# Kernel optimization log

Hardware: AMD Instinct MI355X
Metric: run time of the kernel (lower is better)

## Reference

```python
import jax, jax.numpy as jnp
import numpy as np

EPS_BN = 1e-5
K_NN = 5


def _curvature(x, k=K_NN):
    # x: [B, P, 3] -> concat inverse mean kNN distance -> [B, P, 4]
    def per_sample(pts):  # [P, 3]
        sq = jnp.sum(pts * pts, axis=1)
        d2 = sq[:, None] + sq[None, :] - 2.0 * (pts @ pts.T)
        dist = jnp.sqrt(jnp.maximum(d2, 0.0))  # [P, P], matches torch.cdist p=2
        neg_vals, _ = jax.lax.top_k(-dist, k + 1)  # k+1 smallest distances
        dists = -neg_vals[:, 1:]  # drop self (distance 0)
        dmean = jnp.mean(dists, axis=1, keepdims=True)  # [P, 1]
        return 1.0 / (1e-8 + dmean)
    curv = jax.vmap(per_sample)(x)  # [B, P, 1]
    return jnp.concatenate([x, curv], axis=2)


def _bn(h, g, b, axes):
    # BatchNorm (training mode, batch statistics), biased variance like torch
    m = jnp.mean(h, axis=axes, keepdims=True)
    v = jnp.var(h, axis=axes, keepdims=True)
    return (h - m) / jnp.sqrt(v + EPS_BN) * g + b


def setup_inputs() -> dict:
    key = jax.random.key(0)
    ks = jax.random.split(key, 16)
    B, P, OUTDIM = 32, 2048, 40

    def rn(k, shape, scale=0.05):
        return jax.random.normal(k, shape, dtype=jnp.float32) * scale

    return {
        "x": jax.random.normal(ks[0], (B, P, 3), dtype=jnp.float32),
        # 1x1 Conv1d weights stored as [out_ch, in_ch]
        "conv1_w": rn(ks[1], (64, 4)), "conv1_b": rn(ks[2], (64,)),
        "bn1_g": jnp.ones((64,), jnp.float32), "bn1_b": jnp.zeros((64,), jnp.float32),
        "conv2_w": rn(ks[3], (128, 64)), "conv2_b": rn(ks[4], (128,)),
        "bn2_g": jnp.ones((128,), jnp.float32), "bn2_b": jnp.zeros((128,), jnp.float32),
        "conv3_w": rn(ks[5], (1024, 128)), "conv3_b": rn(ks[6], (1024,)),
        "bn3_g": jnp.ones((1024,), jnp.float32), "bn3_b": jnp.zeros((1024,), jnp.float32),
        "fc1_w": rn(ks[7], (512, 1024)), "fc1_b": rn(ks[8], (512,)),
        "bnf1_g": jnp.ones((512,), jnp.float32), "bnf1_b": jnp.zeros((512,), jnp.float32),
        "fc2_w": rn(ks[9], (256, 512)), "fc2_b": rn(ks[10], (256,)),
        "bnf2_g": jnp.ones((256,), jnp.float32), "bnf2_b": jnp.zeros((256,), jnp.float32),
        # outdim separate Linear(256,1) layers stacked into one [OUTDIM, 256] matrix
        "out_w": rn(ks[11], (OUTDIM, 256)), "out_b": rn(ks[12], (OUTDIM,)),
    }


def reference(x, conv1_w, conv1_b, bn1_g, bn1_b, conv2_w, conv2_b, bn2_g, bn2_b,
              conv3_w, conv3_b, bn3_g, bn3_b, fc1_w, fc1_b, bnf1_g, bnf1_b,
              fc2_w, fc2_b, bnf2_g, bnf2_b, out_w, out_b):
    h = _curvature(x)  # [B, P, 4]
    # feature_layer1: Conv1d(4,64,1)+BN+ReLU; 1x1 conv == per-point matmul
    h = jax.nn.relu(_bn(h @ conv1_w.T + conv1_b, bn1_g, bn1_b, (0, 1)))
    # feature_layer2: Conv1d(64,128,1)+BN+ReLU, Conv1d(128,1024,1)+BN+ReLU
    h = jax.nn.relu(_bn(h @ conv2_w.T + conv2_b, bn2_g, bn2_b, (0, 1)))
    h = jax.nn.relu(_bn(h @ conv3_w.T + conv3_b, bn3_g, bn3_b, (0, 1)))
    h = jnp.max(h, axis=1)  # global max pool over points -> [B, 1024]
    # shared_layer
    h = jax.nn.relu(_bn(h @ fc1_w.T + fc1_b, bnf1_g, bnf1_b, (0,)))
    h = jax.nn.relu(_bn(h @ fc2_w.T + fc2_b, bnf2_g, bnf2_b, (0,)))
    logits = h @ out_w.T + out_b  # concatenated per-class Linear(256,1) heads
    return jax.nn.log_softmax(logits, axis=1)
```

## Files before the change

kernel.cpp:

```cpp
#include <hip/hip_runtime.h>
#include <hip/hip_bf16.h>
#include <math.h>

#define EPS_BN 1e-5f

constexpr int BATCH = 32;
constexpr int NPTS  = 2048;
constexpr int BP    = BATCH * NPTS;

using s16x8 = __attribute__((ext_vector_type(8))) short;
using u32x4 = __attribute__((ext_vector_type(4))) unsigned;
using f32x4 = __attribute__((ext_vector_type(4))) float;

static __device__ __forceinline__ unsigned short f2bf(float f) {
  union { float f; unsigned u; } x{f};
  unsigned r = x.u + 0x7fffu + ((x.u >> 16) & 1u);
  return (unsigned short)(r >> 16);
}
static __device__ __forceinline__ float bf2f(unsigned short s) {
  union { unsigned u; float f; } x;
  x.u = ((unsigned)s) << 16;
  return x.f;
}
static __device__ __forceinline__ unsigned pk2bf(float lo, float hi) {
  __hip_bfloat162 t = __float22bfloat162_rn(float2{lo, hi});
  unsigned r;
  __builtin_memcpy(&r, &t, 4);
  return r;
}

static __device__ __forceinline__ void gload_lds16(const void* g, void* l) {
  __builtin_amdgcn_global_load_lds((const __attribute__((address_space(1))) void*)g,
                                   (__attribute__((address_space(3))) void*)l, 16, 0, 0);
}

static __device__ __forceinline__ float wave_reduce_add(float v) {
#pragma unroll
  for (int off = 32; off > 0; off >>= 1) v += __shfl_xor(v, off);
  return v;
}

static __device__ __forceinline__ void ins6(float (&nn)[6], float c) {
  float b0 = fminf(nn[0], c);
  float b1 = __builtin_amdgcn_fmed3f(c, nn[1], nn[0]);
  float b2 = __builtin_amdgcn_fmed3f(c, nn[2], nn[1]);
  float b3 = __builtin_amdgcn_fmed3f(c, nn[3], nn[2]);
  float b4 = __builtin_amdgcn_fmed3f(c, nn[4], nn[3]);
  float b5 = __builtin_amdgcn_fmed3f(c, nn[5], nn[4]);
  nn[0] = b0; nn[1] = b1; nn[2] = b2; nn[3] = b3; nn[4] = b4; nn[5] = b5;
}

constexpr int CHP = 257;
__global__ __launch_bounds__(256) void curv1_kernel(const float* __restrict__ x,
                                                    const float* __restrict__ c1w,
                                                    const float* __restrict__ c1b,
                                                    unsigned short* __restrict__ z1bf,
                                                    float* __restrict__ part) {
  __shared__ float4 pts[8 * CHP];
  __shared__ float wT[4 * 64], lb1[64], sfeat[32 * 4];
  __shared__ float ls[256], lq[256];
  int b = blockIdx.y;
  const float* xb = x + (size_t)b * NPTS * 3;
  int tid = threadIdx.x;
  {
    int k = tid >> 6, c = tid & 63;
    wT[k * 64 + c] = c1w[c * 4 + k];
    if (tid < 64) lb1[tid] = c1b[tid];
  }
#pragma unroll
  for (int k = 0; k < 8; k++) {
    int i = k * 256 + tid;
    float qx = xb[i * 3 + 0], qy = xb[i * 3 + 1], qz = xb[i * 3 + 2];
    pts[k * CHP + tid] = make_float4(qx, qy, qz, 0.5f * (qx * qx + qy * qy + qz * qz));
  }
  __syncthreads();
  int row = blockIdx.x * 32 + (tid >> 3);
  int sub = tid & 7;
  float4 p = pts[(row >> 8) * CHP + (row & 255)];
  float px = p.x, py = p.y, pz = p.z;
  float nn[6];
#pragma unroll
  for (int j = 0; j < 6; j++) nn[j] = 3.4e38f;
  const float4* cp = pts + sub * CHP;
  for (int j = 0; j < 256; j += 4) {
    float4 q0 = cp[j + 0], q1 = cp[j + 1], q2 = cp[j + 2], q3 = cp[j + 3];
    ins6(nn, fmaf(-px, q0.x, fmaf(-py, q0.y, fmaf(-pz, q0.z, q0.w))));
    ins6(nn, fmaf(-px, q1.x, fmaf(-py, q1.y, fmaf(-pz, q1.z, q1.w))));
    ins6(nn, fmaf(-px, q2.x, fmaf(-py, q2.y, fmaf(-pz, q2.z, q2.w))));
    ins6(nn, fmaf(-px, q3.x, fmaf(-py, q3.y, fmaf(-pz, q3.z, q3.w))));
  }
#pragma unroll
  for (int m = 1; m <= 4; m <<= 1) {
    float other[6];
#pragma unroll
    for (int k = 0; k < 6; k++) other[k] = __shfl_xor(nn[k], m);
#pragma unroll
    for (int k = 0; k < 6; k++) ins6(nn, other[k]);
  }
  if (sub == 0) {
    float p2 = px * px + py * py + pz * pz;
    float dm = 0.f;
#pragma unroll
    for (int i = 1; i < 6; i++) dm += sqrtf(fmaxf(fmaf(2.f, nn[i], p2), 0.f));
    dm *= 0.2f;
    float curv = 1.0f / (1e-8f + dm);
    int lr = tid >> 3;
    sfeat[lr * 4 + 0] = px;
    sfeat[lr * 4 + 1] = py;
    sfeat[lr * 4 + 2] = pz;
    sfeat[lr * 4 + 3] = curv;
  }
  __syncthreads();
  {
    int c = tid & 63, rg = tid >> 6;
    float w0 = wT[c], w1 = wT[64 + c], w2v = wT[128 + c], w3 = wT[192 + c];
    float bb = lb1[c];
    int growbase = b * NPTS + blockIdx.x * 32;
    float s = 0.f, q = 0.f;
#pragma unroll
    for (int i = 0; i < 8; i++) {
      int lr = rg * 8 + i;
      float4 f = *(const float4*)(sfeat + lr * 4);
      float acc = bb + f.x * w0 + f.y * w1 + f.z * w2v + f.w * w3;
      s += acc;
      q += acc * acc;
      z1bf[(size_t)(growbase + lr) * 64 + c] = f2bf(acc);
    }
    ls[tid] = s;
    lq[tid] = q;
  }
  __syncthreads();
  if (tid < 64) {
    float ss = 0.f, qq = 0.f;
#pragma unroll
    for (int i = 0; i < 4; i++) { ss += ls[i * 64 + tid]; qq += lq[i * 64 + tid]; }
    size_t bid = (size_t)b * 64 + blockIdx.x;
    part[(bid * 64 + tid) * 2 + 0] = ss;
    part[(bid * 64 + tid) * 2 + 1] = qq;
  }
}

template <int C, int P>
__global__ __launch_bounds__(256) void bnfinP_kernel(const float* __restrict__ part,
                                                     const float* __restrict__ g,
                                                     const float* __restrict__ be,
                                                     float* __restrict__ scale,
                                                     float* __restrict__ shift) {
  int c = blockIdx.x, tid = threadIdx.x;
  float s = 0.f, q = 0.f;
  for (int i = tid; i < P; i += 256) {
    s += part[((size_t)i * C + c) * 2 + 0];
    q += part[((size_t)i * C + c) * 2 + 1];
  }
  __shared__ float ls[256], lq[256];
  ls[tid] = s; lq[tid] = q;
  __syncthreads();
  for (int off = 128; off > 0; off >>= 1) {
    if (tid < off) { ls[tid] += ls[tid + off]; lq[tid] += lq[tid + off]; }
    __syncthreads();
  }
  if (tid == 0) {
    float m = ls[0] * (1.0f / 65536.0f);
    float v = lq[0] * (1.0f / 65536.0f) - m * m;
    float a = g[c] / sqrtf(v + EPS_BN);
    scale[c] = a;
    shift[c] = be[c] - m * a;
  }
}

__global__ __launch_bounds__(256) void wconv_kernel(const float* __restrict__ w3,
                                                    const float* __restrict__ w2,
                                                    unsigned short* __restrict__ w3bf,
                                                    unsigned short* __restrict__ w2bf) {
  int g = blockIdx.x * 256 + threadIdx.x;
  if (blockIdx.x < 128) {
    const float4 v = ((const float4*)w3)[g];
    unsigned short* d = w3bf + (size_t)g * 4;
    d[0] = f2bf(v.x); d[1] = f2bf(v.y); d[2] = f2bf(v.z); d[3] = f2bf(v.w);
  } else {
    int gg = g - 128 * 256;
    const float4 v = ((const float4*)w2)[gg];
    unsigned short* d = w2bf + (size_t)gg * 4;
    d[0] = f2bf(v.x); d[1] = f2bf(v.y); d[2] = f2bf(v.z); d[3] = f2bf(v.w);
  }
}

__global__ __launch_bounds__(256) void gemm2_mfma_kernel(const unsigned short* __restrict__ z1bf,
                                                         const float* __restrict__ s1,
                                                         const float* __restrict__ h1,
                                                         const unsigned short* __restrict__ w2bf,
                                                         const float* __restrict__ bias2,
                                                         unsigned short* __restrict__ z2bf,
                                                         float* __restrict__ part2) {
  __shared__ char lds[33280];
  float* ls1 = (float*)(lds + 32768);
  float* lh1 = ls1 + 64;
  int tid = threadIdx.x;
  int row0 = blockIdx.x * 128;
  if (tid < 64) { ls1[tid] = s1[tid]; lh1[tid] = h1[tid]; }

  s16x8 araw[4], braw[4];
#pragma unroll
  for (int i = 0; i < 4; i++) {
    int L = tid + 256 * i;
    araw[i] = *(const s16x8*)(z1bf + (size_t)row0 * 64 + (size_t)L * 8);
    braw[i] = *(const s16x8*)(w2bf + (size_t)L * 8);
  }
  __syncthreads();

#pragma unroll
  for (int i = 0; i < 4; i++) {
    int L = tid + 256 * i;
    int row = L >> 3, grp = L & 7, k0 = grp * 8;
    float4 sA = *(const float4*)(ls1 + k0);
    float4 sB = *(const float4*)(ls1 + k0 + 4);
    float4 hA = *(const float4*)(lh1 + k0);
    float4 hB = *(const float4*)(lh1 + k0 + 4);
    float v0 = fmaxf(bf2f((unsigned short)araw[i][0]) * sA.x + hA.x, 0.f);
    float v1 = fmaxf(bf2f((unsigned short)araw[i][1]) * sA.y + hA.y, 0.f);
    float v2 = fmaxf(bf2f((unsigned short)araw[i][2]) * sA.z + hA.z, 0.f);
    float v3 = fmaxf(bf2f((unsigned short)araw[i][3]) * sA.w + hA.w, 0.f);
    float v4 = fmaxf(bf2f((unsigned short)araw[i][4]) * sB.x + hB.x, 0.f);
    float v5 = fmaxf(bf2f((unsigned short)araw[i][5]) * sB.y + hB.y, 0.f);
    float v6 = fmaxf(bf2f((unsigned short)araw[i][6]) * sB.z + hB.z, 0.f);
    float v7 = fmaxf(bf2f((unsigned short)araw[i][7]) * sB.w + hB.w, 0.f);
    u32x4 pa = {pk2bf(v0, v1), pk2bf(v2, v3), pk2bf(v4, v5), pk2bf(v6, v7)};
    *(u32x4*)(lds + row * 128 + ((grp ^ (row & 7)) << 4)) = pa;
    *(s16x8*)(lds + 16384 + row * 128 + ((grp ^ (row & 7)) << 4)) = braw[i];
  }
  __syncthreads();

  int w = tid >> 6, lane = tid & 63;
  int wm = w >> 1, wn = w & 1;
  int lrow = lane & 15, lg = lane >> 4;
  int sw = (lrow & 7) << 4;
  f32x4 acc[4][4] = {};
#pragma unroll
  for (int kstep = 0; kstep < 2; kstep++) {
    s16x8 a[4], bfr[4];
#pragma unroll
    for (int m = 0; m < 4; m++) {
      int row = wm * 64 + m * 16 + lrow;
      int byte = row * 128 + ((kstep * 64 + lg * 16) ^ sw);
      a[m] = *(const s16x8*)(lds + byte);
    }
#pragma unroll
    for (int n = 0; n < 4; n++) {
      int col = wn * 64 + n * 16 + lrow;
      int byte = 16384 + col * 128 + ((kstep * 64 + lg * 16) ^ sw);
      bfr[n] = *(const s16x8*)(lds + byte);
    }
#pragma unroll
    for (int m = 0; m < 4; m++)
#pragma unroll
      for (int n = 0; n < 4; n++)
        acc[m][n] = __builtin_amdgcn_mfma_f32_16x16x32_bf16(a[m], bfr[n], acc[m][n], 0, 0, 0);
  }
  __syncthreads();

  float* sS = (float*)lds;
  float* sQ = sS + 256;
#pragma unroll
  for (int n = 0; n < 4; n++) {
    int col = wn * 64 + n * 16 + lrow;
    float bb = bias2[col];
    float s = 0.f, q = 0.f;
#pragma unroll
    for (int m = 0; m < 4; m++) {
#pragma unroll
      for (int r = 0; r < 4; r++) {
        float v = acc[m][n][r] + bb;
        s += v;
        q += v * v;
        int row = row0 + wm * 64 + m * 16 + lg * 4 + r;
        z2bf[(size_t)row * 128 + col] = f2bf(v);
      }
    }
    s += __shfl_xor(s, 16); s += __shfl_xor(s, 32);
    q += __shfl_xor(q, 16); q += __shfl_xor(q, 32);
    if (lane < 16) {
      int cidx = wn * 64 + n * 16 + lane;
      sS[wm * 128 + cidx] = s;
      sQ[wm * 128 + cidx] = q;
    }
  }
  __syncthreads();
  if (tid < 128) {
    part2[((size_t)blockIdx.x * 128 + tid) * 2 + 0] = sS[tid] + sS[128 + tid];
    part2[((size_t)blockIdx.x * 128 + tid) * 2 + 1] = sQ[tid] + sQ[128 + tid];
  }
}

__global__ __launch_bounds__(256) void gemm3_mfma_kernel(const unsigned short* __restrict__ z2bf,
                                                         const float* __restrict__ s2,
                                                         const float* __restrict__ h2,
                                                         const unsigned short* __restrict__ wbf,
                                                         const float* __restrict__ bias3,
                                                         float* __restrict__ pS,
                                                         float* __restrict__ pQ,
                                                         float* __restrict__ pMx,
                                                         float* __restrict__ pMn) {
  __shared__ char lds[70656];
  float* ls2 = (float*)(lds + 69632);
  float* lh2 = ls2 + 128;
  int tid = threadIdx.x;
  int w = tid >> 6, lane = tid & 63;
  int bid = blockIdx.x;
  int rblk = (bid & 7) * 64 + (bid >> 3);
  int row0 = rblk * 128;

  if (tid < 128) { ls2[tid] = s2[tid]; lh2[tid] = h2[tid]; }
  s16x8 araw[8];
#pragma unroll
  for (int i = 0; i < 8; i++) {
    int L = tid + 256 * i;
    int row = L >> 4, gc = L & 15;
    araw[i] = *(const s16x8*)(z2bf + (size_t)(row0 + row) * 128 + gc * 8);
  }
  __syncthreads();
#pragma unroll
  for (int i = 0; i < 8; i++) {
    int L = tid + 256 * i;
    int row = L >> 4, gc = L & 15, k0 = gc * 8;
    float4 sA = *(const float4*)(ls2 + k0);
    float4 sB = *(const float4*)(ls2 + k0 + 4);
    float4 hA = *(const float4*)(lh2 + k0);
    float4 hB = *(const float4*)(lh2 + k0 + 4);
    float v0 = fmaxf(bf2f((unsigned short)araw[i][0]) * sA.x + hA.x, 0.f);
    float v1 = fmaxf(bf2f((unsigned short)araw[i][1]) * sA.y + hA.y, 0.f);
    float v2 = fmaxf(bf2f((unsigned short)araw[i][2]) * sA.z + hA.z, 0.f);
    float v3 = fmaxf(bf2f((unsigned short)araw[i][3]) * sA.w + hA.w, 0.f);
    float v4 = fmaxf(bf2f((unsigned short)araw[i][4]) * sB.x + hB.x, 0.f);
    float v5 = fmaxf(bf2f((unsigned short)araw[i][5]) * sB.y + hB.y, 0.f);
    float v6 = fmaxf(bf2f((unsigned short)araw[i][6]) * sB.z + hB.z, 0.f);
    float v7 = fmaxf(bf2f((unsigned short)araw[i][7]) * sB.w + hB.w, 0.f);
    u32x4 pa = {pk2bf(v0, v1), pk2bf(v2, v3), pk2bf(v4, v5), pk2bf(v6, v7)};
    *(u32x4*)(lds + row * 256 + ((gc ^ (row & 7)) << 4)) = pa;
  }

  int wm = w >> 1, wn = w & 1;
  int lrow = lane & 15, lg = lane >> 4;
  int sw = (lrow & 7) << 4;
  float* sS = (float*)(lds + 65536);
  float* sQ = sS + 256;
  float* sMx = sQ + 256;
  float* sMn = sMx + 256;

  for (int cblk = 0; cblk < 8; cblk++) {
    int col0 = cblk * 128;
#pragma unroll
    for (int i = 0; i < 8; i++) {
      int ldsoff = w * 8192 + i * 1024;
      int lin = ldsoff + lane * 16;
      int row = lin >> 8;
      int gc = (lin >> 4) & 15;
      int gcl = gc ^ (row & 7);
      gload_lds16(wbf + (size_t)(col0 + row) * 128 + gcl * 8, &lds[32768 + ldsoff]);
    }
    __syncthreads();

    f32x4 acc[4][4] = {};
#pragma unroll
    for (int kstep = 0; kstep < 4; kstep++) {
      s16x8 a[4], b[4];
#pragma unroll
      for (int m = 0; m < 4; m++) {
        int row = wm * 64 + m * 16 + lrow;
        int byte = row * 256 + ((kstep * 64 + lg * 16) ^ sw);
        a[m] = *(const s16x8*)(lds + byte);
      }
#pragma unroll
      for (int n = 0; n < 4; n++) {
        int col = wn * 64 + n * 16 + lrow;
        int byte = 32768 + col * 256 + ((kstep * 64 + lg * 16) ^ sw);
        b[n] = *(const s16x8*)(lds + byte);
      }
#pragma unroll
      for (int m = 0; m < 4; m++)
#pragma unroll
        for (int n = 0; n < 4; n++)
          acc[m][n] = __builtin_amdgcn_mfma_f32_16x16x32_bf16(a[m], b[n], acc[m][n], 0, 0, 0);
    }

#pragma unroll
    for (int n = 0; n < 4; n++) {
      float s = 0.f, q = 0.f, mx = -3.4e38f, mn = 3.4e38f;
#pragma unroll
      for (int m = 0; m < 4; m++)
#pragma unroll
        for (int r = 0; r < 4; r++) {
          float v = acc[m][n][r];
          s += v;
          q = fmaf(v, v, q);
          mx = fmaxf(mx, v);
          mn = fminf(mn, v);
        }
      s += __shfl_xor(s, 16); s += __shfl_xor(s, 32);
      q += __shfl_xor(q, 16); q += __shfl_xor(q, 32);
      mx = fmaxf(mx, __shfl_xor(mx, 16)); mx = fmaxf(mx, __shfl_xor(mx, 32));
      mn = fminf(mn, __shfl_xor(mn, 16)); mn = fminf(mn, __shfl_xor(mn, 32));
      if (lane < 16) {
        int cidx = wn * 64 + n * 16 + lane;
        sS[wm * 128 + cidx] = s;
        sQ[wm * 128 + cidx] = q;
        sMx[wm * 128 + cidx] = mx;
        sMn[wm * 128 + cidx] = mn;
      }
    }
    __syncthreads();
    if (tid < 128) {
      float bcol = bias3[col0 + tid];
      float S = sS[tid] + sS[128 + tid];
      float Q = sQ[tid] + sQ[128 + tid];
      size_t o = (size_t)rblk * 1024 + col0 + tid;
      pS[o] = S + 128.f * bcol;
      pQ[o] = Q + 2.f * bcol * S + 128.f * bcol * bcol;
      pMx[o] = fmaxf(sMx[tid], sMx[128 + tid]) + bcol;
      pMn[o] = fminf(sMn[tid], sMn[128 + tid]) + bcol;
    }
    __syncthreads();
  }
}

__global__ __launch_bounds__(256) void bn3fin_pool_kernel(const float* __restrict__ pS,
                                                          const float* __restrict__ pQ,
                                                          const float* __restrict__ pMx,
                                                          const float* __restrict__ pMn,
                                                          const float* __restrict__ g,
                                                          const float* __restrict__ be,
                                                          float* __restrict__ pooled) {
  int tid = threadIdx.x;
  int chl = tid & 15, grp = tid >> 4;
  int c = blockIdx.x * 16 + chl;
  float s = 0.f, q = 0.f;
  for (int i = grp; i < 512; i += 16) {
    s += pS[(size_t)i * 1024 + c];
    q += pQ[(size_t)i * 1024 + c];
  }
  __shared__ float ls[256], lq[256], sa[16], sc[16];
  ls[chl * 16 + grp] = s;
  lq[chl * 16 + grp] = q;
  __syncthreads();
  if (tid < 16) {
    float ss = 0.f, qq = 0.f;
#pragma unroll
    for (int i = 0; i < 16; i++) { ss += ls[tid * 16 + i]; qq += lq[tid * 16 + i]; }
    float m = ss * (1.0f / 65536.0f);
    float v = qq * (1.0f / 65536.0f) - m * m;
    float a = g[blockIdx.x * 16 + tid] / sqrtf(v + EPS_BN);
    sa[tid] = a;
    sc[tid] = be[blockIdx.x * 16 + tid] - m * a;
  }
  __syncthreads();
  for (int idx = tid; idx < 512; idx += 256) {
    int b = idx >> 4, l = idx & 15;
    int cc = blockIdx.x * 16 + l;
    float mx = -3.4e38f, mn = 3.4e38f;
    for (int i = 0; i < 16; i++) {
      mx = fmaxf(mx, pMx[(size_t)(b * 16 + i) * 1024 + cc]);
      mn = fminf(mn, pMn[(size_t)(b * 16 + i) * 1024 + cc]);
    }
    float a = sa[l];
    float v = (a > 0.f) ? (a * mx + sc[l]) : (a * mn + sc[l]);
    pooled[(size_t)b * 1024 + cc] = fmaxf(v, 0.f);
  }
}

__global__ __launch_bounds__(256) void fc1_kernel(const float* __restrict__ pooled,
                                                  const float* __restrict__ w,
                                                  const float* __restrict__ bias,
                                                  float* __restrict__ zf1) {
  int gw = blockIdx.x * 4 + (threadIdx.x >> 6);
  int lane = threadIdx.x & 63;
  int b = gw >> 9, o = gw & 511;
  const float4* pr = (const float4*)(pooled + (size_t)b * 1024);
  const float4* wr = (const float4*)(w + (size_t)o * 1024);
  float acc = 0.f;
#pragma unroll
  for (int i = 0; i < 4; i++) {
    int k = lane + i * 64;
    float4 p = pr[k], q = wr[k];
    acc += p.x * q.x + p.y * q.y + p.z * q.z + p.w * q.w;
  }
  acc = wave_reduce_add(acc);
  if (lane == 0) zf1[gw] = acc + bias[o];
}

__global__ __launch_bounds__(256) void statsF_kernel(const float* __restrict__ z,
                                                     const float* __restrict__ g,
                                                     const float* __restrict__ be, int C,
                                                     float* __restrict__ scale,
                                                     float* __restrict__ shift) {
  int c = blockIdx.x * 256 + threadIdx.x;
  if (c >= C) return;
  float s = 0.f, q = 0.f;
  for (int b = 0; b < 32; b++) {
    float v = z[(size_t)b * C + c];
    s += v;
    q += v * v;
  }
  float m = s * (1.0f / 32.0f);
  float v = q * (1.0f / 32.0f) - m * m;
  float a = g[c] / sqrtf(v + EPS_BN);
  scale[c] = a;
  shift[c] = be[c] - m * a;
}

__global__ __launch_bounds__(256) void fc2_kernel(const float* __restrict__ zf1,
                                                  const float* __restrict__ sf1,
                                                  const float* __restrict__ hf1,
                                                  const float* __restrict__ w,
                                                  const float* __restrict__ bias,
                                                  float* __restrict__ zf2) {
  int gw = blockIdx.x * 4 + (threadIdx.x >> 6);
  int lane = threadIdx.x & 63;
  int b = gw >> 8, o = gw & 255;
  const float4* zr = (const float4*)(zf1 + (size_t)b * 512);
  const float4* sr = (const float4*)sf1;
  const float4* hr = (const float4*)hf1;
  const float4* wr = (const float4*)(w + (size_t)o * 512);
  float acc = 0.f;
#pragma unroll
  for (int i = 0; i < 2; i++) {
    int k = lane + i * 64;
    float4 z = zr[k], s = sr[k], h = hr[k], q = wr[k];
    float v0 = fmaxf(z.x * s.x + h.x, 0.f);
    float v1 = fmaxf(z.y * s.y + h.y, 0.f);
    float v2 = fmaxf(z.z * s.z + h.z, 0.f);
    float v3 = fmaxf(z.w * s.w + h.w, 0.f);
    acc += v0 * q.x + v1 * q.y + v2 * q.z + v3 * q.w;
  }
  acc = wave_reduce_add(acc);
  if (lane == 0) zf2[gw] = acc + bias[o];
}

__global__ __launch_bounds__(256) void head_kernel(const float* __restrict__ zf2,
                                                   const float* __restrict__ gf2,
                                                   const float* __restrict__ bef2,
                                                   const float* __restrict__ w,
                                                   const float* __restrict__ bias,
                                                   float* __restrict__ out) {
  int b = blockIdx.x, tid = threadIdx.x;
  int wv = tid >> 6, lane = tid & 63;
  __shared__ float ssf[256], shf[256], lg[40], red[2];
  {
    float s = 0.f, q = 0.f;
    for (int bb = 0; bb < 32; bb++) {
      float v = zf2[(size_t)bb * 256 + tid];
      s += v;
      q += v * v;
    }
    float m = s * (1.0f / 32.0f);
    float var = q * (1.0f / 32.0f) - m * m;
    float a = gf2[tid] / sqrtf(var + EPS_BN);
    ssf[tid] = a;
    shf[tid] = bef2[tid] - m * a;
  }
  __syncthreads();
  float4 z = ((const float4*)(zf2 + (size_t)b * 256))[lane];
  float4 s = ((const float4*)ssf)[lane];
  float4 h = ((const float4*)shf)[lane];
  float v0 = fmaxf(z.x * s.x + h.x, 0.f);
  float v1 = fmaxf(z.y * s.y + h.y, 0.f);
  float v2 = fmaxf(z.z * s.z + h.z, 0.f);
  float v3 = fmaxf(z.w * s.w + h.w, 0.f);
  for (int r = 0; r < 10; r++) {
    int o = wv * 10 + r;
    float4 q = ((const float4*)(w + (size_t)o * 256))[lane];
    float a = v0 * q.x + v1 * q.y + v2 * q.z + v3 * q.w;
    a = wave_reduce_add(a);
    if (lane == 0) lg[o] = a + bias[o];
  }
  __syncthreads();
  if (tid == 0) {
    float mx = -3.4e38f;
    for (int i = 0; i < 40; i++) mx = fmaxf(mx, lg[i]);
    float sum = 0.f;
    for (int i = 0; i < 40; i++) sum += expf(lg[i] - mx);
    red[0] = mx;
    red[1] = logf(sum);
  }
  __syncthreads();
  if (tid < 40) out[(size_t)b * 40 + tid] = lg[tid] - red[0] - red[1];
}

extern "C" void kernel_launch(void* const* d_in, const int* in_sizes, int n_in,
                              void* d_out, int out_size, void* d_ws, size_t ws_size,
                              hipStream_t stream) {
  const float* x    = (const float*)d_in[0];
  const float* c1w  = (const float*)d_in[1];
  const float* c1b  = (const float*)d_in[2];
  const float* g1   = (const float*)d_in[3];
  const float* be1  = (const float*)d_in[4];
  const float* c2w  = (const float*)d_in[5];
  const float* c2b  = (const float*)d_in[6];
  const float* g2   = (const float*)d_in[7];
  const float* be2  = (const float*)d_in[8];
  const float* c3w  = (const float*)d_in[9];
  const float* c3b  = (const float*)d_in[10];
  const float* g3   = (const float*)d_in[11];
  const float* be3  = (const float*)d_in[12];
  const float* f1w  = (const float*)d_in[13];
  const float* f1b  = (const float*)d_in[14];
  const float* gf1  = (const float*)d_in[15];
  const float* bef1 = (const float*)d_in[16];
  const float* f2w  = (const float*)d_in[17];
  const float* f2b  = (const float*)d_in[18];
  const float* gf2  = (const float*)d_in[19];
  const float* bef2 = (const float*)d_in[20];
  const float* ow   = (const float*)d_in[21];
  const float* ob   = (const float*)d_in[22];
  float* out = (float*)d_out;

  float* W = (float*)d_ws;
  float* pS     = W;
  float* pQ     = pS + 524288;
  float* pMx    = pQ + 524288;
  float* pMn    = pMx + 524288;
  float* part   = pMn + 524288;
  float* part2  = part + 262144;
  float* pooled = part2 + 131072;
  float* zf1    = pooled + 32768;
  float* zf2    = zf1 + 16384;
  float* s1     = zf2 + 8192;
  float* h1     = s1 + 64;
  float* s2     = h1 + 64;
  float* h2     = s2 + 128;
  float* sf1    = h2 + 128;
  float* hf1    = sf1 + 512;
  unsigned short* wbf  = (unsigned short*)(hf1 + 512);
  unsigned short* w2bf = wbf + 131072;
  unsigned short* z1bf = w2bf + 8192;
  unsigned short* z2bf = z1bf + (size_t)BP * 64;

  wconv_kernel<<<136, 256, 0, stream>>>(c3w, c2w, wbf, w2bf);
  curv1_kernel<<<dim3(64, 32), 256, 0, stream>>>(x, c1w, c1b, z1bf, part);
  bnfinP_kernel<64, 2048><<<64, 256, 0, stream>>>(part, g1, be1, s1, h1);
  gemm2_mfma_kernel<<<512, 256, 0, stream>>>(z1bf, s1, h1, w2bf, c2b, z2bf, part2);
  bnfinP_kernel<128, 512><<<128, 256, 0, stream>>>(part2, g2, be2, s2, h2);
  gemm3_mfma_kernel<<<512, 256, 0, stream>>>(z2bf, s2, h2, wbf, c3b, pS, pQ, pMx, pMn);
  bn3fin_pool_kernel<<<64, 256, 0, stream>>>(pS, pQ, pMx, pMn, g3, be3, pooled);
  fc1_kernel<<<4096, 256, 0, stream>>>(pooled, f1w, f1b, zf1);
  statsF_kernel<<<2, 256, 0, stream>>>(zf1, gf1, bef1, 512, sf1, hf1);
  fc2_kernel<<<2048, 256, 0, stream>>>(zf1, sf1, hf1, f2w, f2b, zf2);
  head_kernel<<<32, 256, 0, stream>>>(zf2, gf2, bef2, ow, ob, out);
}
```

Before: 130.0 us.

## Fold weight conversion into curvature kernel, prefetch kNN loads, tree-reduce min/max

Removes the separate weight-to-bf16 conversion kernel by adding an extra row of blocks to the curvature kernel that converts conv3 and conv2 weights with vectorized stores. This saves one launch and its serialization on the stream. The kNN inner loop now register-double-buffers eight LDS points per step so loads overlap the insertion network. The gemm3 epilogue computes max and min with a tree instead of a serial chain to shorten dependency depth, at the cost of more live registers.

```diff
diff --git a/kernel.cpp b/kernel.cpp
--- a/kernel.cpp
+++ b/kernel.cpp
@@ -9,6 +9,7 @@
 constexpr int BP    = BATCH * NPTS;
 
 using s16x8 = __attribute__((ext_vector_type(8))) short;
+using u16x4 = __attribute__((ext_vector_type(4))) unsigned short;
 using u32x4 = __attribute__((ext_vector_type(4))) unsigned;
 using f32x4 = __attribute__((ext_vector_type(4))) float;
 
@@ -54,8 +55,29 @@
 __global__ __launch_bounds__(256) void curv1_kernel(const float* __restrict__ x,
                                                     const float* __restrict__ c1w,
                                                     const float* __restrict__ c1b,
+                                                    const float* __restrict__ w3,
+                                                    const float* __restrict__ w2,
+                                                    unsigned short* __restrict__ w3bf,
+                                                    unsigned short* __restrict__ w2bf,
                                                     unsigned short* __restrict__ z1bf,
                                                     float* __restrict__ part) {
+  if (blockIdx.y == 32) {
+    int g = blockIdx.x * 256 + threadIdx.x;
+    {
+      const float4 v0 = ((const float4*)w3)[g];
+      const float4 v1 = ((const float4*)w3)[g + 16384];
+      u16x4 a{f2bf(v0.x), f2bf(v0.y), f2bf(v0.z), f2bf(v0.w)};
+      u16x4 b{f2bf(v1.x), f2bf(v1.y), f2bf(v1.z), f2bf(v1.w)};
+      *(u16x4*)(w3bf + (size_t)g * 4) = a;
+      *(u16x4*)(w3bf + (size_t)(g + 16384) * 4) = b;
+    }
+    if (g < 2048) {
+      const float4 v = ((const float4*)w2)[g];
+      u16x4 a{f2bf(v.x), f2bf(v.y), f2bf(v.z), f2bf(v.w)};
+      *(u16x4*)(w2bf + (size_t)g * 4) = a;
+    }
+    return;
+  }
   __shared__ float4 pts[8 * CHP];
   __shared__ float wT[4 * 64], lb1[64], sfeat[32 * 4];
   __shared__ float ls[256], lq[256];
@@ -82,13 +104,22 @@
 #pragma unroll
   for (int j = 0; j < 6; j++) nn[j] = 3.4e38f;
   const float4* cp = pts + sub * CHP;
-  for (int j = 0; j < 256; j += 4) {
-    float4 q0 = cp[j + 0], q1 = cp[j + 1], q2 = cp[j + 2], q3 = cp[j + 3];
-    ins6(nn, fmaf(-px, q0.x, fmaf(-py, q0.y, fmaf(-pz, q0.z, q0.w))));
-    ins6(nn, fmaf(-px, q1.x, fmaf(-py, q1.y, fmaf(-pz, q1.z, q1.w))));
-    ins6(nn, fmaf(-px, q2.x, fmaf(-py, q2.y, fmaf(-pz, q2.z, q2.w))));
-    ins6(nn, fmaf(-px, q3.x, fmaf(-py, q3.y, fmaf(-pz, q3.z, q3.w))));
-  }
+  float4 buf[8];
+#pragma unroll
+  for (int t = 0; t < 8; t++) buf[t] = cp[t];
+  for (int j = 8; j < 256; j += 8) {
+    float4 nxt[8];
+#pragma unroll
+    for (int t = 0; t < 8; t++) nxt[t] = cp[j + t];
+#pragma unroll
+    for (int t = 0; t < 8; t++)
+      ins6(nn, fmaf(-px, buf[t].x, fmaf(-py, buf[t].y, fmaf(-pz, buf[t].z, buf[t].w))));
+#pragma unroll
+    for (int t = 0; t < 8; t++) buf[t] = nxt[t];
+  }
+#pragma unroll
+  for (int t = 0; t < 8; t++)
+    ins6(nn, fmaf(-px, buf[t].x, fmaf(-py, buf[t].y, fmaf(-pz, buf[t].z, buf[t].w))));
 #pragma unroll
   for (int m = 1; m <= 4; m <<= 1) {
     float other[6];
@@ -113,7 +144,7 @@
   __syncthreads();
   {
     int c = tid & 63, rg = tid >> 6;
-    float w0 = wT[c], w1 = wT[64 + c], w2v = wT[128 + c], w3 = wT[192 + c];
+    float w0 = wT[c], w1 = wT[64 + c], w2v = wT[128 + c], w3v = wT[192 + c];
     float bb = lb1[c];
     int growbase = b * NPTS + blockIdx.x * 32;
     float s = 0.f, q = 0.f;
@@ -121,7 +152,7 @@
     for (int i = 0; i < 8; i++) {
       int lr = rg * 8 + i;
       float4 f = *(const float4*)(sfeat + lr * 4);
-      float acc = bb + f.x * w0 + f.y * w1 + f.z * w2v + f.w * w3;
+      float acc = bb + f.x * w0 + f.y * w1 + f.z * w2v + f.w * w3v;
       s += acc;
       q += acc * acc;
       z1bf[(size_t)(growbase + lr) * 64 + c] = f2bf(acc);
@@ -165,23 +196,6 @@
     float a = g[c] / sqrtf(v + EPS_BN);
     scale[c] = a;
     shift[c] = be[c] - m * a;
-  }
-}
-
-__global__ __launch_bounds__(256) void wconv_kernel(const float* __restrict__ w3,
-                                                    const float* __restrict__ w2,
-                                                    unsigned short* __restrict__ w3bf,
-                                                    unsigned short* __restrict__ w2bf) {
-  int g = blockIdx.x * 256 + threadIdx.x;
-  if (blockIdx.x < 128) {
-    const float4 v = ((const float4*)w3)[g];
-    unsigned short* d = w3bf + (size_t)g * 4;
-    d[0] = f2bf(v.x); d[1] = f2bf(v.y); d[2] = f2bf(v.z); d[3] = f2bf(v.w);
-  } else {
-    int gg = g - 128 * 256;
-    const float4 v = ((const float4*)w2)[gg];
-    unsigned short* d = w2bf + (size_t)gg * 4;
-    d[0] = f2bf(v.x); d[1] = f2bf(v.y); d[2] = f2bf(v.z); d[3] = f2bf(v.w);
   }
 }
 
@@ -384,17 +398,27 @@
 
 #pragma unroll
     for (int n = 0; n < 4; n++) {
-      float s = 0.f, q = 0.f, mx = -3.4e38f, mn = 3.4e38f;
+      float v[16];
+      float s = 0.f, q = 0.f;
 #pragma unroll
       for (int m = 0; m < 4; m++)
 #pragma unroll
         for (int r = 0; r < 4; r++) {
-          float v = acc[m][n][r];
-          s += v;
-          q = fmaf(v, v, q);
-          mx = fmaxf(mx, v);
-          mn = fminf(mn, v);
+          float t = acc[m][n][r];
+          v[m * 4 + r] = t;
+          s += t;
+          q = fmaf(t, t, q);
         }
+      float mx = fmaxf(fmaxf(fmaxf(fmaxf(v[0], v[1]), v[2]),
+                             fmaxf(fmaxf(v[3], v[4]), v[5])),
+                       fmaxf(fmaxf(fmaxf(v[6], v[7]), v[8]),
+                             fmaxf(fmaxf(v[9], v[10]), v[11])));
+      mx = fmaxf(mx, fmaxf(fmaxf(v[12], v[13]), fmaxf(v[14], v[15])));
+      float mn = fminf(fminf(fminf(fminf(v[0], v[1]), v[2]),
+                             fminf(fminf(v[3], v[4]), v[5])),
+                       fminf(fminf(fminf(v[6], v[7]), v[8]),
+                             fminf(fminf(v[9], v[10]), v[11])));
+      mn = fminf(mn, fminf(fminf(v[12], v[13]), fminf(v[14], v[15])));
       s += __shfl_xor(s, 16); s += __shfl_xor(s, 32);
       q += __shfl_xor(q, 16); q += __shfl_xor(q, 32);
       mx = fmaxf(mx, __shfl_xor(mx, 16)); mx = fmaxf(mx, __shfl_xor(mx, 32));
@@ -633,8 +657,7 @@
   unsigned short* z1bf = w2bf + 8192;
   unsigned short* z2bf = z1bf + (size_t)BP * 64;
 
-  wconv_kernel<<<136, 256, 0, stream>>>(c3w, c2w, wbf, w2bf);
-  curv1_kernel<<<dim3(64, 32), 256, 0, stream>>>(x, c1w, c1b, z1bf, part);
+  curv1_kernel<<<dim3(64, 33), 256, 0, stream>>>(x, c1w, c1b, c3w, c2w, wbf, w2bf, z1bf, part);
   bnfinP_kernel<64, 2048><<<64, 256, 0, stream>>>(part, g1, be1, s1, h1);
   gemm2_mfma_kernel<<<512, 256, 0, stream>>>(z1bf, s1, h1, w2bf, c2b, z2bf, part2);
   bnfinP_kernel<128, 512><<<128, 256, 0, stream>>>(part2, g2, be2, s2, h2);
```

After: 132.7 us. 1.02x slower.
